# Optimization experiments

Measured on AMD Instinct MI355X. Metric: run time of the kernel, lower is better.

## Reference

```python
import jax, jax.numpy as jnp
import numpy as np

INPT, HID, NNODE, K, B = 64, 128, 10000, 16, 8

def setup_inputs() -> dict:
    key = jax.random.key(0)
    ks = jax.random.split(key, 12)
    def lin(k, fan_in, fan_out):
        # orthogonal-ish init stand-in; exact init values are irrelevant for the reference math
        return jax.random.normal(k, (fan_in, fan_out), jnp.float32) / np.sqrt(fan_in)
    return {
        "state": jax.random.normal(ks[0], (B, NNODE, INPT), jnp.float32),
        "internal": jax.random.normal(ks[1], (B, NNODE, INPT), jnp.float32),
        "state_neigh": jax.random.randint(ks[2], (NNODE, K), 0, NNODE),
        "internal_neigh": jax.random.randint(ks[3], (NNODE, K), 0, NNODE),
        "W1": lin(ks[4], INPT, HID), "b1": jnp.zeros((HID,), jnp.float32),
        "W2": lin(ks[5], HID, HID), "b2": jnp.zeros((HID,), jnp.float32),
        "Wu1": lin(ks[6], 2 * HID, HID), "bu1": jnp.zeros((HID,), jnp.float32),
        "Wu2": lin(ks[7], 2 * HID, HID), "bu2": jnp.zeros((HID,), jnp.float32),
    }

def _aggregate(se, ie, s_idx, i_idx):
    # se, ie: [B, N, H]; idx: [N, K] -> gather neighbors and sum over K
    g_s = jnp.take(se, s_idx, axis=1).sum(axis=2)   # [B, N, H]
    g_i = jnp.take(ie, i_idx, axis=1).sum(axis=2)   # [B, N, H]
    return g_s + g_i

def _update(aggr, h, W, b):
    x = jnp.concatenate((aggr, h), axis=-1)          # [B, N, 2H]
    return jax.nn.relu(x @ W + b)

def reference(state, internal, state_neigh, internal_neigh,
              W1, b1, W2, b2, Wu1, bu1, Wu2, bu2):
    # layer-1 embeddings
    state_embed = jax.nn.relu(state @ W1 + b1)       # [B, N, H]
    internal_embed = jax.nn.relu(internal @ W1 + b1)
    aggr1 = _aggregate(state_embed, internal_embed, state_neigh, internal_neigh)
    hu1 = _update(aggr1, internal_embed, Wu1, bu1)   # [B, N, H]
    # layer-2 embeddings
    se2 = jax.nn.relu(state_embed @ W2 + b2)
    ie2 = jax.nn.relu(hu1 @ W2 + b2)
    aggr2 = _aggregate(se2, ie2, state_neigh, internal_neigh)
    hu2 = _update(aggr2, ie2, Wu2, bu2)              # [B, N, H]
    return hu1, hu2
```

## Files before the change

kernel.cpp:

```cpp
#include <hip/hip_runtime.h>

#define HID 128
#define NNODE 10000
#define KN 16
#define ROWS 80000
#define NTILES 2500
#define ANCH 313

typedef __attribute__((ext_vector_type(8))) short short8;
typedef __attribute__((ext_vector_type(4))) float f32x4;
typedef __attribute__((ext_vector_type(2))) float f32x2;
typedef __attribute__((ext_vector_type(2))) unsigned int u32x2;

__device__ __forceinline__ unsigned short f2b(float f) {
    unsigned u = __float_as_uint(f);
    u += 0x7FFFu + ((u >> 16) & 1u);
    return (unsigned short)(u >> 16);
}

__global__ __launch_bounds__(256) void wconv_all(
    const float* __restrict__ W1, const float* __restrict__ W2,
    const float* __restrict__ Wu1, const float* __restrict__ Wu2,
    unsigned short* __restrict__ W1t, unsigned short* __restrict__ W2t,
    unsigned short* __restrict__ Wu1t, unsigned short* __restrict__ Wu2t) {
    int idx = blockIdx.x * 256 + threadIdx.x;
    const float* W; unsigned short* Wt; int K; int off;
    if (idx < 8192)       { W = W1;  Wt = W1t;  K = 64;  off = idx; }
    else if (idx < 24576) { W = W2;  Wt = W2t;  K = 128; off = idx - 8192; }
    else if (idx < 57344) { W = Wu1; Wt = Wu1t; K = 256; off = idx - 24576; }
    else                  { W = Wu2; Wt = Wu2t; K = 256; off = idx - 57344; }
    int n = off & 127, k = off >> 7;
    Wt[n * K + k] = f2b(W[off]);
}

template<int K, bool AF32>
__global__ __launch_bounds__(512) void embed2(
    const void* __restrict__ A0, const void* __restrict__ A1,
    const unsigned short* __restrict__ Wt, const float* __restrict__ bias,
    unsigned short* __restrict__ Y0, unsigned short* __restrict__ Y1, int tot) {
    const int t = threadIdx.x, w = t >> 6, lane = t & 63;
    const int lrow = lane & 15, lk = lane >> 4;
    const int rs = w & 1, ng = w >> 1;
    const int col0 = ng * 32;

    short8 wf[2][K / 32];
    f32x4 bv[2];
#pragma unroll
    for (int p = 0; p < 2; ++p) {
        bv[p] = *(const f32x4*)(bias + col0 + p * 16 + lk * 4);
#pragma unroll
        for (int kt = 0; kt < K / 32; ++kt)
            wf[p][kt] = *(const short8*)(Wt + (col0 + p * 16 + lrow) * K + kt * 32 + lk * 8);
    }

    int T = blockIdx.x;
    if (T >= tot) return;

    auto loadx = [&](int TT, short8* xf) {
        const int half = TT >= NTILES;
        const void* A = half ? A1 : A0;
        const int row = (TT - half * NTILES) * 32 + rs * 16 + lrow;
        if constexpr (AF32) {
            const float* X = (const float*)A + (size_t)row * K;
#pragma unroll
            for (int kt = 0; kt < K / 32; ++kt) {
                f32x4 f0 = *(const f32x4*)(X + kt * 32 + lk * 8);
                f32x4 f1 = *(const f32x4*)(X + kt * 32 + lk * 8 + 4);
                short8 v;
#pragma unroll
                for (int e = 0; e < 4; ++e) { v[e] = (short)f2b(f0[e]); v[4 + e] = (short)f2b(f1[e]); }
                xf[kt] = v;
            }
        } else {
            const unsigned short* X = (const unsigned short*)A + (size_t)row * K;
#pragma unroll
            for (int kt = 0; kt < K / 32; ++kt)
                xf[kt] = *(const short8*)(X + kt * 32 + lk * 8);
        }
    };

    short8 xf[K / 32], xn[K / 32];
    loadx(T, xf);
    for (;;) {
        const int Tn = T + gridDim.x;
        const bool more = Tn < tot;
        if (more) loadx(Tn, xn);

        const int half = T >= NTILES;
        unsigned short* Y = half ? Y1 : Y0;
        const int row = (T - half * NTILES) * 32 + rs * 16 + lrow;
#pragma unroll
        for (int p = 0; p < 2; ++p) {
            f32x4 acc = {0.f, 0.f, 0.f, 0.f};
#pragma unroll
            for (int kt = 0; kt < K / 32; ++kt)
                acc = __builtin_amdgcn_mfma_f32_16x16x32_bf16(wf[p][kt], xf[kt], acc, 0, 0, 0);
            float v0 = acc[0] + bv[p][0]; v0 = v0 > 0.f ? v0 : 0.f;
            float v1 = acc[1] + bv[p][1]; v1 = v1 > 0.f ? v1 : 0.f;
            float v2 = acc[2] + bv[p][2]; v2 = v2 > 0.f ? v2 : 0.f;
            float v3 = acc[3] + bv[p][3]; v3 = v3 > 0.f ? v3 : 0.f;
            u32x2 ov = {(unsigned)f2b(v0) | ((unsigned)f2b(v1) << 16),
                        (unsigned)f2b(v2) | ((unsigned)f2b(v3) << 16)};
            *(u32x2*)(Y + (size_t)row * HID + col0 + p * 16 + lk * 4) = ov;
        }
        if (!more) break;
#pragma unroll
        for (int kt = 0; kt < K / 32; ++kt) xf[kt] = xn[kt];
        T = Tn;
    }
}

__global__ __launch_bounds__(512) void aggr3(
    const unsigned short* __restrict__ SE, const unsigned short* __restrict__ IE,
    const int* __restrict__ sidx, const int* __restrict__ iidx,
    unsigned short* __restrict__ G) {
    __shared__ int sh[32][33];
    const int t = threadIdx.x;
    const int b = blockIdx.x & 7;
    const int hc = blockIdx.x >> 3;
    const int h = hc >= ANCH ? 1 : 0;
    const int c = hc - h * ANCH;
    const int n0 = c * 32;

#pragma unroll
    for (int q = 0; q < 2; ++q) {
        const int e = t + q * 512;
        const int r = e >> 5, k = e & 31;
        int nr = n0 + r; if (nr > NNODE - 1) nr = NNODE - 1;
        sh[r][k] = (k < KN) ? sidx[nr * KN + k] : iidx[nr * KN + (k - KN)];
    }
    __syncthreads();

    const int r = t >> 4, p = t & 15;
    const int col0 = h * 64 + p * 4;
    const int n = n0 + r;
    const size_t base = (size_t)b * NNODE * HID + col0;

    u32x2 vs[16], vi[16];
#pragma unroll
    for (int j = 0; j < 16; ++j)
        vs[j] = *(const u32x2*)(SE + base + (size_t)sh[r][j] * HID);
#pragma unroll
    for (int j = 0; j < 16; ++j)
        vi[j] = *(const u32x2*)(IE + base + (size_t)sh[r][16 + j] * HID);

    f32x2 a0 = {0.f, 0.f}, a1 = {0.f, 0.f};
#pragma unroll
    for (int j = 0; j < 16; ++j) {
        unsigned u0 = vs[j][0], u1 = vs[j][1];
        a0 += (f32x2){__uint_as_float(u0 << 16), __uint_as_float(u0 & 0xffff0000u)};
        a1 += (f32x2){__uint_as_float(u1 << 16), __uint_as_float(u1 & 0xffff0000u)};
    }
#pragma unroll
    for (int j = 0; j < 16; ++j) {
        unsigned u0 = vi[j][0], u1 = vi[j][1];
        a0 += (f32x2){__uint_as_float(u0 << 16), __uint_as_float(u0 & 0xffff0000u)};
        a1 += (f32x2){__uint_as_float(u1 << 16), __uint_as_float(u1 & 0xffff0000u)};
    }

    if (n < NNODE) {
        u32x2 ov = {(unsigned)f2b(a0.x) | ((unsigned)f2b(a0.y) << 16),
                    (unsigned)f2b(a1.x) | ((unsigned)f2b(a1.y) << 16)};
        *(u32x2*)(G + ((size_t)b * NNODE + n) * HID + col0) = ov;
    }
}

__global__ __launch_bounds__(512) void update_gemm2(
    const unsigned short* __restrict__ G, const unsigned short* __restrict__ H,
    const unsigned short* __restrict__ Wut, const float* __restrict__ bu,
    float* __restrict__ Yf, unsigned short* __restrict__ Yb, int writeb) {
    const int t = threadIdx.x, w = t >> 6, lane = t & 63;
    const int lrow = lane & 15, lk = lane >> 4;
    const int rs = w & 1, ng = w >> 1;
    const int col0 = ng * 32;

    short8 wf[2][8];
    f32x4 bv[2];
#pragma unroll
    for (int p = 0; p < 2; ++p) {
        bv[p] = *(const f32x4*)(bu + col0 + p * 16 + lk * 4);
#pragma unroll
        for (int kt = 0; kt < 8; ++kt)
            wf[p][kt] = *(const short8*)(Wut + (col0 + p * 16 + lrow) * 256 + kt * 32 + lk * 8);
    }

    for (int T = blockIdx.x; T < NTILES; T += gridDim.x) {
        const int row = T * 32 + rs * 16 + lrow;
        short8 xf[8];
#pragma unroll
        for (int kt = 0; kt < 4; ++kt) {
            xf[kt]     = *(const short8*)(G + (size_t)row * HID + kt * 32 + lk * 8);
            xf[4 + kt] = *(const short8*)(H + (size_t)row * HID + kt * 32 + lk * 8);
        }
#pragma unroll
        for (int p = 0; p < 2; ++p) {
            f32x4 acc = {0.f, 0.f, 0.f, 0.f};
#pragma unroll
            for (int kt = 0; kt < 8; ++kt)
                acc = __builtin_amdgcn_mfma_f32_16x16x32_bf16(wf[p][kt], xf[kt], acc, 0, 0, 0);
            f32x4 o;
#pragma unroll
            for (int j = 0; j < 4; ++j) {
                float v = acc[j] + bv[p][j];
                o[j] = v > 0.f ? v : 0.f;
            }
            *(f32x4*)(Yf + (size_t)row * HID + col0 + p * 16 + lk * 4) = o;
            if (writeb) {
                u32x2 ov = {(unsigned)f2b(o[0]) | ((unsigned)f2b(o[1]) << 16),
                            (unsigned)f2b(o[2]) | ((unsigned)f2b(o[3]) << 16)};
                *(u32x2*)(Yb + (size_t)row * HID + col0 + p * 16 + lk * 4) = ov;
            }
        }
    }
}

extern "C" void kernel_launch(void* const* d_in, const int* in_sizes, int n_in,
                              void* d_out, int out_size, void* d_ws, size_t ws_size,
                              hipStream_t stream) {
    const float* state    = (const float*)d_in[0];
    const float* internal = (const float*)d_in[1];
    const int*   sidx     = (const int*)d_in[2];
    const int*   iidx     = (const int*)d_in[3];
    const float* W1  = (const float*)d_in[4];
    const float* b1  = (const float*)d_in[5];
    const float* W2  = (const float*)d_in[6];
    const float* b2  = (const float*)d_in[7];
    const float* Wu1 = (const float*)d_in[8];
    const float* bu1 = (const float*)d_in[9];
    const float* Wu2 = (const float*)d_in[10];
    const float* bu2 = (const float*)d_in[11];

    float* hu1 = (float*)d_out;
    float* hu2 = hu1 + (size_t)ROWS * HID;

    unsigned short* W1t  = (unsigned short*)d_ws;
    unsigned short* W2t  = W1t  + 64 * 128;
    unsigned short* Wu1t = W2t  + 128 * 128;
    unsigned short* Wu2t = Wu1t + 256 * 128;
    unsigned short* bufA = Wu2t + 256 * 128;
    unsigned short* bufB = bufA + (size_t)ROWS * HID;
    unsigned short* bufC = bufB + (size_t)ROWS * HID;
    unsigned short* bufD = bufC + (size_t)ROWS * HID;

    const size_t need4 = (size_t)90112 * 2 + 4 * (size_t)ROWS * HID * 2;
    const bool big = ws_size >= need4;

    dim3 b256(256), b512(512);
    const int AGRID = 8 * 2 * ANCH;

    wconv_all<<<352, b256, 0, stream>>>(W1, W2, Wu1, Wu2, W1t, W2t, Wu1t, Wu2t);

    embed2<64, true><<<1250, b512, 0, stream>>>(state, internal, W1t, b1, bufA, bufB, 2 * NTILES);

    if (big) {
        aggr3<<<AGRID, b512, 0, stream>>>(bufA, bufB, sidx, iidx, bufD);
        update_gemm2<<<1250, b512, 0, stream>>>(bufD, bufB, Wu1t, bu1, hu1, bufC, 1);
        embed2<128, false><<<1250, b512, 0, stream>>>(bufA, bufC, W2t, b2, bufB, bufD, 2 * NTILES);
        aggr3<<<AGRID, b512, 0, stream>>>(bufB, bufD, sidx, iidx, bufA);
        update_gemm2<<<1250, b512, 0, stream>>>(bufA, bufD, Wu2t, bu2, hu2, nullptr, 0);
    } else {
        unsigned short* Ghu2 = (unsigned short*)hu2;
        aggr3<<<AGRID, b512, 0, stream>>>(bufA, bufB, sidx, iidx, Ghu2);
        update_gemm2<<<1250, b512, 0, stream>>>(Ghu2, bufB, Wu1t, bu1, hu1, bufC, 1);
        embed2<128, false><<<1250, b512, 0, stream>>>(bufA, nullptr, W2t, b2, bufB, nullptr, NTILES);
        embed2<128, false><<<1250, b512, 0, stream>>>(bufC, nullptr, W2t, b2, bufA, nullptr, NTILES);
        aggr3<<<AGRID, b512, 0, stream>>>(bufB, bufA, sidx, iidx, bufC);
        update_gemm2<<<1250, b512, 0, stream>>>(bufC, bufA, Wu2t, bu2, hu2, nullptr, 0);
    }
}
```

Before: 235.5 us.

## Fuse layer-2 embedding GEMM into embed1 and update1 kernels via LDS

The W2 embedding GEMM is folded into the producers of its inputs. The first-layer embed kernel also computes se2 for the state half. The first update kernel computes ie2 directly from hu1. Both stage the bf16 tile in an XOR-swizzled LDS buffer to re-layout it as MFMA operands. This drops a separate kernel launch and the global write/read round-trip of bf16 hu1 and the re-read of SE1. It also interleaves load and accumulate in the aggregation kernel to cut register pressure. The trade-offs: the embed kernel loses its software prefetch of the next tile, two __syncthreads are added per tile, and W2 fragments are reloaded from global/cache every tile.

Measured after the change: 237.9 us. Within noise of the previous version (+1.0%).

```diff
diff --git a/kernel.cpp b/kernel.cpp
--- a/kernel.cpp
+++ b/kernel.cpp
@@ -6,6 +6,7 @@
 #define ROWS 80000
 #define NTILES 2500
 #define ANCH 313
+#define AGRID (8 * 2 * ANCH)
 
 typedef __attribute__((ext_vector_type(8))) short short8;
 typedef __attribute__((ext_vector_type(4))) float f32x4;
@@ -33,84 +34,98 @@
     Wt[n * K + k] = f2b(W[off]);
 }
 
-template<int K, bool AF32>
-__global__ __launch_bounds__(512) void embed2(
-    const void* __restrict__ A0, const void* __restrict__ A1,
-    const unsigned short* __restrict__ Wt, const float* __restrict__ bias,
-    unsigned short* __restrict__ Y0, unsigned short* __restrict__ Y1, int tot) {
+__device__ __forceinline__ void lds_write8(unsigned short* Yt, int row, int bc, u32x2 v) {
+    *(u32x2*)((char*)Yt + row * 256 + (bc ^ ((row & 7) << 4))) = v;
+}
+__device__ __forceinline__ short8 lds_read16(const unsigned short* Yt, int row, int bc) {
+    return *(const short8*)((const char*)Yt + row * 256 + (bc ^ ((row & 7) << 4)));
+}
+
+__global__ __launch_bounds__(512) void k_embed1_fused(
+    const float* __restrict__ state, const float* __restrict__ internal,
+    const unsigned short* __restrict__ W1t, const float* __restrict__ b1,
+    const unsigned short* __restrict__ W2t, const float* __restrict__ b2,
+    unsigned short* __restrict__ SE1, unsigned short* __restrict__ IE1,
+    unsigned short* __restrict__ se2) {
+    __shared__ __align__(16) unsigned short Yt[32 * 128];
     const int t = threadIdx.x, w = t >> 6, lane = t & 63;
     const int lrow = lane & 15, lk = lane >> 4;
     const int rs = w & 1, ng = w >> 1;
     const int col0 = ng * 32;
-
-    short8 wf[2][K / 32];
-    f32x4 bv[2];
+    const int row_l = rs * 16 + lrow;
+
+    short8 wf[2][2];
+    f32x4 bv1[2], bv2[2];
 #pragma unroll
     for (int p = 0; p < 2; ++p) {
-        bv[p] = *(const f32x4*)(bias + col0 + p * 16 + lk * 4);
-#pragma unroll
-        for (int kt = 0; kt < K / 32; ++kt)
-            wf[p][kt] = *(const short8*)(Wt + (col0 + p * 16 + lrow) * K + kt * 32 + lk * 8);
-    }
-
-    int T = blockIdx.x;
-    if (T >= tot) return;
-
-    auto loadx = [&](int TT, short8* xf) {
-        const int half = TT >= NTILES;
-        const void* A = half ? A1 : A0;
-        const int row = (TT - half * NTILES) * 32 + rs * 16 + lrow;
-        if constexpr (AF32) {
-            const float* X = (const float*)A + (size_t)row * K;
-#pragma unroll
-            for (int kt = 0; kt < K / 32; ++kt) {
-                f32x4 f0 = *(const f32x4*)(X + kt * 32 + lk * 8);
-                f32x4 f1 = *(const f32x4*)(X + kt * 32 + lk * 8 + 4);
-                short8 v;
-#pragma unroll
-                for (int e = 0; e < 4; ++e) { v[e] = (short)f2b(f0[e]); v[4 + e] = (short)f2b(f1[e]); }
-                xf[kt] = v;
-            }
-        } else {
-            const unsigned short* X = (const unsigned short*)A + (size_t)row * K;
-#pragma unroll
-            for (int kt = 0; kt < K / 32; ++kt)
-                xf[kt] = *(const short8*)(X + kt * 32 + lk * 8);
-        }
-    };
-
-    short8 xf[K / 32], xn[K / 32];
-    loadx(T, xf);
-    for (;;) {
-        const int Tn = T + gridDim.x;
-        const bool more = Tn < tot;
-        if (more) loadx(Tn, xn);
-
+        bv1[p] = *(const f32x4*)(b1 + col0 + p * 16 + lk * 4);
+        bv2[p] = *(const f32x4*)(b2 + col0 + p * 16 + lk * 4);
+#pragma unroll
+        for (int kt = 0; kt < 2; ++kt)
+            wf[p][kt] = *(const short8*)(W1t + (col0 + p * 16 + lrow) * 64 + kt * 32 + lk * 8);
+    }
+
+    for (int T = blockIdx.x; T < 2 * NTILES; T += 1250) {
         const int half = T >= NTILES;
-        unsigned short* Y = half ? Y1 : Y0;
-        const int row = (T - half * NTILES) * 32 + rs * 16 + lrow;
+        const float* X = half ? internal : state;
+        unsigned short* Y = half ? IE1 : SE1;
+        const int row = (T - half * NTILES) * 32 + row_l;
+
+        short8 xf[2];
+#pragma unroll
+        for (int kt = 0; kt < 2; ++kt) {
+            const float* p4 = X + (size_t)row * 64 + kt * 32 + lk * 8;
+            f32x4 f0 = *(const f32x4*)p4;
+            f32x4 f1 = *(const f32x4*)(p4 + 4);
+            short8 v;
+#pragma unroll
+            for (int e = 0; e < 4; ++e) { v[e] = (short)f2b(f0[e]); v[4 + e] = (short)f2b(f1[e]); }
+            xf[kt] = v;
+        }
+
 #pragma unroll
         for (int p = 0; p < 2; ++p) {
             f32x4 acc = {0.f, 0.f, 0.f, 0.f};
-#pragma unroll
-            for (int kt = 0; kt < K / 32; ++kt)
-                acc = __builtin_amdgcn_mfma_f32_16x16x32_bf16(wf[p][kt], xf[kt], acc, 0, 0, 0);
-            float v0 = acc[0] + bv[p][0]; v0 = v0 > 0.f ? v0 : 0.f;
-            float v1 = acc[1] + bv[p][1]; v1 = v1 > 0.f ? v1 : 0.f;
-            float v2 = acc[2] + bv[p][2]; v2 = v2 > 0.f ? v2 : 0.f;
-            float v3 = acc[3] + bv[p][3]; v3 = v3 > 0.f ? v3 : 0.f;
+            acc = __builtin_amdgcn_mfma_f32_16x16x32_bf16(wf[p][0], xf[0], acc, 0, 0, 0);
+            acc = __builtin_amdgcn_mfma_f32_16x16x32_bf16(wf[p][1], xf[1], acc, 0, 0, 0);
+            float v0 = acc[0] + bv1[p][0]; v0 = v0 > 0.f ? v0 : 0.f;
+            float v1 = acc[1] + bv1[p][1]; v1 = v1 > 0.f ? v1 : 0.f;
+            float v2 = acc[2] + bv1[p][2]; v2 = v2 > 0.f ? v2 : 0.f;
+            float v3 = acc[3] + bv1[p][3]; v3 = v3 > 0.f ? v3 : 0.f;
             u32x2 ov = {(unsigned)f2b(v0) | ((unsigned)f2b(v1) << 16),
                         (unsigned)f2b(v2) | ((unsigned)f2b(v3) << 16)};
             *(u32x2*)(Y + (size_t)row * HID + col0 + p * 16 + lk * 4) = ov;
-        }
-        if (!more) break;
-#pragma unroll
-        for (int kt = 0; kt < K / 32; ++kt) xf[kt] = xn[kt];
-        T = Tn;
-    }
-}
-
-__global__ __launch_bounds__(512) void aggr3(
+            if (!half) lds_write8(Yt, row_l, col0 * 2 + p * 32 + lk * 8, ov);
+        }
+
+        if (!half) {
+            __syncthreads();
+            short8 x2[4];
+#pragma unroll
+            for (int kt = 0; kt < 4; ++kt)
+                x2[kt] = lds_read16(Yt, row_l, kt * 64 + lk * 16);
+            __syncthreads();
+#pragma unroll
+            for (int p = 0; p < 2; ++p) {
+                f32x4 acc = {0.f, 0.f, 0.f, 0.f};
+#pragma unroll
+                for (int kt = 0; kt < 4; ++kt) {
+                    short8 w2f = *(const short8*)(W2t + (col0 + p * 16 + lrow) * 128 + kt * 32 + lk * 8);
+                    acc = __builtin_amdgcn_mfma_f32_16x16x32_bf16(w2f, x2[kt], acc, 0, 0, 0);
+                }
+                float v0 = acc[0] + bv2[p][0]; v0 = v0 > 0.f ? v0 : 0.f;
+                float v1 = acc[1] + bv2[p][1]; v1 = v1 > 0.f ? v1 : 0.f;
+                float v2 = acc[2] + bv2[p][2]; v2 = v2 > 0.f ? v2 : 0.f;
+                float v3 = acc[3] + bv2[p][3]; v3 = v3 > 0.f ? v3 : 0.f;
+                u32x2 ov = {(unsigned)f2b(v0) | ((unsigned)f2b(v1) << 16),
+                            (unsigned)f2b(v2) | ((unsigned)f2b(v3) << 16)};
+                *(u32x2*)(se2 + (size_t)row * HID + col0 + p * 16 + lk * 4) = ov;
+            }
+        }
+    }
+}
+
+__global__ __launch_bounds__(512) void k_aggrD(
     const unsigned short* __restrict__ SE, const unsigned short* __restrict__ IE,
     const int* __restrict__ sidx, const int* __restrict__ iidx,
     unsigned short* __restrict__ G) {
@@ -136,26 +151,30 @@
     const int n = n0 + r;
     const size_t base = (size_t)b * NNODE * HID + col0;
 
-    u32x2 vs[16], vi[16];
-#pragma unroll
-    for (int j = 0; j < 16; ++j)
-        vs[j] = *(const u32x2*)(SE + base + (size_t)sh[r][j] * HID);
-#pragma unroll
-    for (int j = 0; j < 16; ++j)
-        vi[j] = *(const u32x2*)(IE + base + (size_t)sh[r][16 + j] * HID);
-
     f32x2 a0 = {0.f, 0.f}, a1 = {0.f, 0.f};
-#pragma unroll
-    for (int j = 0; j < 16; ++j) {
-        unsigned u0 = vs[j][0], u1 = vs[j][1];
-        a0 += (f32x2){__uint_as_float(u0 << 16), __uint_as_float(u0 & 0xffff0000u)};
-        a1 += (f32x2){__uint_as_float(u1 << 16), __uint_as_float(u1 & 0xffff0000u)};
-    }
-#pragma unroll
-    for (int j = 0; j < 16; ++j) {
-        unsigned u0 = vi[j][0], u1 = vi[j][1];
-        a0 += (f32x2){__uint_as_float(u0 << 16), __uint_as_float(u0 & 0xffff0000u)};
-        a1 += (f32x2){__uint_as_float(u1 << 16), __uint_as_float(u1 & 0xffff0000u)};
+    {
+        u32x2 vs[16];
+#pragma unroll
+        for (int j = 0; j < 16; ++j)
+            vs[j] = *(const u32x2*)(SE + base + (size_t)sh[r][j] * HID);
+#pragma unroll
+        for (int j = 0; j < 16; ++j) {
+            unsigned u0 = vs[j][0], u1 = vs[j][1];
+            a0 += (f32x2){__uint_as_float(u0 << 16), __uint_as_float(u0 & 0xffff0000u)};
+            a1 += (f32x2){__uint_as_float(u1 << 16), __uint_as_float(u1 & 0xffff0000u)};
+        }
+    }
+    {
+        u32x2 vi[16];
+#pragma unroll
+        for (int j = 0; j < 16; ++j)
+            vi[j] = *(const u32x2*)(IE + base + (size_t)sh[r][16 + j] * HID);
+#pragma unroll
+        for (int j = 0; j < 16; ++j) {
+            unsigned u0 = vi[j][0], u1 = vi[j][1];
+            a0 += (f32x2){__uint_as_float(u0 << 16), __uint_as_float(u0 & 0xffff0000u)};
+            a1 += (f32x2){__uint_as_float(u1 << 16), __uint_as_float(u1 & 0xffff0000u)};
+        }
     }
 
     if (n < NNODE) {
@@ -165,10 +184,84 @@
     }
 }
 
-__global__ __launch_bounds__(512) void update_gemm2(
+__global__ __launch_bounds__(512) void k_update1_fused(
+    const unsigned short* __restrict__ G, const unsigned short* __restrict__ H,
+    const unsigned short* __restrict__ Wu1t, const float* __restrict__ bu1,
+    const unsigned short* __restrict__ W2t, const float* __restrict__ b2,
+    float* __restrict__ hu1, unsigned short* __restrict__ ie2) {
+    __shared__ __align__(16) unsigned short Yt[32 * 128];
+    const int t = threadIdx.x, w = t >> 6, lane = t & 63;
+    const int lrow = lane & 15, lk = lane >> 4;
+    const int rs = w & 1, ng = w >> 1;
+    const int col0 = ng * 32;
+    const int row_l = rs * 16 + lrow;
+
+    short8 wf[2][8];
+    f32x4 bv[2], bv2[2];
+#pragma unroll
+    for (int p = 0; p < 2; ++p) {
+        bv[p]  = *(const f32x4*)(bu1 + col0 + p * 16 + lk * 4);
+        bv2[p] = *(const f32x4*)(b2  + col0 + p * 16 + lk * 4);
+#pragma unroll
+        for (int kt = 0; kt < 8; ++kt)
+            wf[p][kt] = *(const short8*)(Wu1t + (col0 + p * 16 + lrow) * 256 + kt * 32 + lk * 8);
+    }
+
+    for (int T = blockIdx.x; T < NTILES; T += 1250) {
+        const int row = T * 32 + row_l;
+        short8 xf[8];
+#pragma unroll
+        for (int kt = 0; kt < 4; ++kt) {
+            xf[kt]     = *(const short8*)(G + (size_t)row * HID + kt * 32 + lk * 8);
+            xf[4 + kt] = *(const short8*)(H + (size_t)row * HID + kt * 32 + lk * 8);
+        }
+#pragma unroll
+        for (int p = 0; p < 2; ++p) {
+            f32x4 acc = {0.f, 0.f, 0.f, 0.f};
+#pragma unroll
+            for (int kt = 0; kt < 8; ++kt)
+                acc = __builtin_amdgcn_mfma_f32_16x16x32_bf16(wf[p][kt], xf[kt], acc, 0, 0, 0);
+            f32x4 o;
+#pragma unroll
+            for (int j = 0; j < 4; ++j) {
+                float v = acc[j] + bv[p][j];
+                o[j] = v > 0.f ? v : 0.f;
+            }
+            *(f32x4*)(hu1 + (size_t)row * HID + col0 + p * 16 + lk * 4) = o;
+            u32x2 ov = {(unsigned)f2b(o[0]) | ((unsigned)f2b(o[1]) << 16),
+                        (unsigned)f2b(o[2]) | ((unsigned)f2b(o[3]) << 16)};
+            lds_write8(Yt, row_l, col0 * 2 + p * 32 + lk * 8, ov);
+        }
+
+        __syncthreads();
+        short8 x2[4];
+#pragma unroll
+        for (int kt = 0; kt < 4; ++kt)
+            x2[kt] = lds_read16(Yt, row_l, kt * 64 + lk * 16);
+        __syncthreads();
+#pragma unroll
+        for (int p = 0; p < 2; ++p) {
+            f32x4 acc = {0.f, 0.f, 0.f, 0.f};
+#pragma unroll
+            for (int kt = 0; kt < 4; ++kt) {
+                short8 w2f = *(const short8*)(W2t + (col0 + p * 16 + lrow) * 128 + kt * 32 + lk * 8);
+                acc = __builtin_amdgcn_mfma_f32_16x16x32_bf16(w2f, x2[kt], acc, 0, 0, 0);
+            }
+            float v0 = acc[0] + bv2[p][0]; v0 = v0 > 0.f ? v0 : 0.f;
+            float v1 = acc[1] + bv2[p][1]; v1 = v1 > 0.f ? v1 : 0.f;
+            float v2 = acc[2] + bv2[p][2]; v2 = v2 > 0.f ? v2 : 0.f;
+            float v3 = acc[3] + bv2[p][3]; v3 = v3 > 0.f ? v3 : 0.f;
+            u32x2 ov = {(unsigned)f2b(v0) | ((unsigned)f2b(v1) << 16),
+                        (unsigned)f2b(v2) | ((unsigned)f2b(v3) << 16)};
+            *(u32x2*)(ie2 + (size_t)row * HID + col0 + p * 16 + lk * 4) = ov;
+        }
+    }
+}
+
+__global__ __launch_bounds__(512) void k_update2(
     const unsigned short* __restrict__ G, const unsigned short* __restrict__ H,
     const unsigned short* __restrict__ Wut, const float* __restrict__ bu,
-    float* __restrict__ Yf, unsigned short* __restrict__ Yb, int writeb) {
+    float* __restrict__ Yf) {
     const int t = threadIdx.x, w = t >> 6, lane = t & 63;
     const int lrow = lane & 15, lk = lane >> 4;
     const int rs = w & 1, ng = w >> 1;
@@ -205,11 +298,6 @@
                 o[j] = v > 0.f ? v : 0.f;
             }
             *(f32x4*)(Yf + (size_t)row * HID + col0 + p * 16 + lk * 4) = o;
-            if (writeb) {
-                u32x2 ov = {(unsigned)f2b(o[0]) | ((unsigned)f2b(o[1]) << 16),
-                            (unsigned)f2b(o[2]) | ((unsigned)f2b(o[3]) << 16)};
-                *(u32x2*)(Yb + (size_t)row * HID + col0 + p * 16 + lk * 4) = ov;
-            }
         }
     }
 }
@@ -234,37 +322,31 @@
     float* hu2 = hu1 + (size_t)ROWS * HID;
 
     unsigned short* W1t  = (unsigned short*)d_ws;
-    unsigned short* W2t  = W1t  + 64 * 128;
-    unsigned short* Wu1t = W2t  + 128 * 128;
-    unsigned short* Wu2t = Wu1t + 256 * 128;
-    unsigned short* bufA = Wu2t + 256 * 128;
-    unsigned short* bufB = bufA + (size_t)ROWS * HID;
-    unsigned short* bufC = bufB + (size_t)ROWS * HID;
-    unsigned short* bufD = bufC + (size_t)ROWS * HID;
-
-    const size_t need4 = (size_t)90112 * 2 + 4 * (size_t)ROWS * HID * 2;
-    const bool big = ws_size >= need4;
+    unsigned short* W2t  = W1t + 8192;
+    unsigned short* Wu1t = W2t + 16384;
+    unsigned short* Wu2t = Wu1t + 32768;
+    unsigned short* buf0 = Wu2t + 32768;
+    unsigned short* buf1 = buf0 + (size_t)ROWS * HID;
+    unsigned short* buf2 = buf1 + (size_t)ROWS * HID;
+    unsigned short* buf3 = buf2 + (size_t)ROWS * HID;
+
+    const size_t need_big = ((size_t)90112 + 4 * (size_t)ROWS * HID) * 2;
+    const bool big = ws_size >= need_big;
 
     dim3 b256(256), b512(512);
-    const int AGRID = 8 * 2 * ANCH;
 
     wconv_all<<<352, b256, 0, stream>>>(W1, W2, Wu1, Wu2, W1t, W2t, Wu1t, Wu2t);
 
-    embed2<64, true><<<1250, b512, 0, stream>>>(state, internal, W1t, b1, bufA, bufB, 2 * NTILES);
-
-    if (big) {
-        aggr3<<<AGRID, b512, 0, stream>>>(bufA, bufB, sidx, iidx, bufD);
-        update_gemm2<<<1250, b512, 0, stream>>>(bufD, bufB, Wu1t, bu1, hu1, bufC, 1);
-        embed2<128, false><<<1250, b512, 0, stream>>>(bufA, bufC, W2t, b2, bufB, bufD, 2 * NTILES);
-        aggr3<<<AGRID, b512, 0, stream>>>(bufB, bufD, sidx, iidx, bufA);
-        update_gemm2<<<1250, b512, 0, stream>>>(bufA, bufD, Wu2t, bu2, hu2, nullptr, 0);
-    } else {
-        unsigned short* Ghu2 = (unsigned short*)hu2;
-        aggr3<<<AGRID, b512, 0, stream>>>(bufA, bufB, sidx, iidx, Ghu2);
-        update_gemm2<<<1250, b512, 0, stream>>>(Ghu2, bufB, Wu1t, bu1, hu1, bufC, 1);
-        embed2<128, false><<<1250, b512, 0, stream>>>(bufA, nullptr, W2t, b2, bufB, nullptr, NTILES);
-        embed2<128, false><<<1250, b512, 0, stream>>>(bufC, nullptr, W2t, b2, bufA, nullptr, NTILES);
-        aggr3<<<AGRID, b512, 0, stream>>>(bufB, bufA, sidx, iidx, bufC);
-        update_gemm2<<<1250, b512, 0, stream>>>(bufC, bufA, Wu2t, bu2, hu2, nullptr, 0);
-    }
-}
+    k_embed1_fused<<<1250, b512, 0, stream>>>(state, internal, W1t, b1, W2t, b2,
+                                              buf0, buf1, buf2);
+
+    unsigned short* G1 = big ? buf3 : (unsigned short*)hu2;
+
+    k_aggrD<<<AGRID, b512, 0, stream>>>(buf0, buf1, sidx, iidx, G1);
+
+    k_update1_fused<<<1250, b512, 0, stream>>>(G1, buf1, Wu1t, bu1, W2t, b2, hu1, buf0);
+
+    k_aggrD<<<AGRID, b512, 0, stream>>>(buf2, buf0, sidx, iidx, buf1);
+
+    k_update2<<<1250, b512, 0, stream>>>(buf1, buf0, Wu2t, bu2, hu2);
+}
```

## Stage neighbor gathers through LDS via direct global-to-LDS loads; prefetch update tiles

Applied to the files above, without the earlier changes.

Rewrites the aggregation kernel so the neighbor rows are copied straight into shared memory with global_load_lds. Each wave loads 4 neighbors across 8 row-pairs, the work runs in two phases of 16 nodes, and the sum is then read back from LDS per thread. The update GEMM gains software prefetching of the next tile's inputs and launches with half as many blocks, so each block processes two tiles. The aim is to raise memory-level parallelism in the gather and hide load latency in the GEMM, at the cost of 64KB of LDS per block and fewer resident blocks.

New measurement: 251.1 us. 1.07x slower.

```diff
diff --git a/kernel.cpp b/kernel.cpp
--- a/kernel.cpp
+++ b/kernel.cpp
@@ -6,10 +6,10 @@
 #define ROWS 80000
 #define NTILES 2500
 #define ANCH 313
+#define AGRID (8 * 2 * ANCH)
 
 typedef __attribute__((ext_vector_type(8))) short short8;
 typedef __attribute__((ext_vector_type(4))) float f32x4;
-typedef __attribute__((ext_vector_type(2))) float f32x2;
 typedef __attribute__((ext_vector_type(2))) unsigned int u32x2;
 
 __device__ __forceinline__ unsigned short f2b(float f) {
@@ -110,17 +110,21 @@
     }
 }
 
-__global__ __launch_bounds__(512) void aggr3(
+__global__ __launch_bounds__(512) void k_aggrL(
     const unsigned short* __restrict__ SE, const unsigned short* __restrict__ IE,
     const int* __restrict__ sidx, const int* __restrict__ iidx,
     unsigned short* __restrict__ G) {
     __shared__ int sh[32][33];
+    __shared__ __align__(16) unsigned short stage[8 * 32 * 2 * 64];
     const int t = threadIdx.x;
+    const int lane = t & 63, wv = t >> 6;
     const int b = blockIdx.x & 7;
     const int hc = blockIdx.x >> 3;
     const int h = hc >= ANCH ? 1 : 0;
     const int c = hc - h * ANCH;
     const int n0 = c * 32;
+    const size_t gbase = (size_t)b * NNODE * HID;
+    const int colbase = h * 64;
 
 #pragma unroll
     for (int q = 0; q < 2; ++q) {
@@ -131,37 +135,44 @@
     }
     __syncthreads();
 
-    const int r = t >> 4, p = t & 15;
-    const int col0 = h * 64 + p * 4;
-    const int n = n0 + r;
-    const size_t base = (size_t)b * NNODE * HID + col0;
-
-    u32x2 vs[16], vi[16];
-#pragma unroll
-    for (int j = 0; j < 16; ++j)
-        vs[j] = *(const u32x2*)(SE + base + (size_t)sh[r][j] * HID);
-#pragma unroll
-    for (int j = 0; j < 16; ++j)
-        vi[j] = *(const u32x2*)(IE + base + (size_t)sh[r][16 + j] * HID);
-
-    f32x2 a0 = {0.f, 0.f}, a1 = {0.f, 0.f};
-#pragma unroll
-    for (int j = 0; j < 16; ++j) {
-        unsigned u0 = vs[j][0], u1 = vs[j][1];
-        a0 += (f32x2){__uint_as_float(u0 << 16), __uint_as_float(u0 & 0xffff0000u)};
-        a1 += (f32x2){__uint_as_float(u1 << 16), __uint_as_float(u1 & 0xffff0000u)};
-    }
-#pragma unroll
-    for (int j = 0; j < 16; ++j) {
-        unsigned u0 = vi[j][0], u1 = vi[j][1];
-        a0 += (f32x2){__uint_as_float(u0 << 16), __uint_as_float(u0 & 0xffff0000u)};
-        a1 += (f32x2){__uint_as_float(u1 << 16), __uint_as_float(u1 & 0xffff0000u)};
-    }
-
-    if (n < NNODE) {
-        u32x2 ov = {(unsigned)f2b(a0.x) | ((unsigned)f2b(a0.y) << 16),
-                    (unsigned)f2b(a1.x) | ((unsigned)f2b(a1.y) << 16)};
-        *(u32x2*)(G + ((size_t)b * NNODE + n) * HID + col0) = ov;
+#pragma unroll
+    for (int ph = 0; ph < 2; ++ph) {
+        {
+            const unsigned short* SRC = (wv < 4) ? SE : IE;
+#pragma unroll
+            for (int pr = 0; pr < 8; ++pr) {
+#pragma unroll
+                for (int j = 0; j < 4; ++j) {
+                    const int nb = wv * 4 + j;
+                    const int rA = ph * 16 + pr * 2 + (lane >> 5);
+                    const int idx = sh[rA][nb];
+                    const unsigned short* gp = SRC + gbase + (size_t)idx * HID
+                                               + colbase + (lane & 31) * 2;
+                    unsigned short* lp = stage + (pr * 32 + nb) * 128;
+                    __builtin_amdgcn_global_load_lds(
+                        (const __attribute__((address_space(1))) void*)gp,
+                        (__attribute__((address_space(3))) void*)lp, 4, 0, 0);
+                }
+            }
+        }
+        __syncthreads();
+
+        const int r = t >> 5, cc = t & 31;
+        const int pr = r >> 1, ro = r & 1;
+        float a0 = 0.f, a1 = 0.f;
+        const unsigned* sp = (const unsigned*)stage + ((size_t)pr * 64 + ro) * 32 + cc;
+#pragma unroll
+        for (int nb = 0; nb < 32; ++nb) {
+            const unsigned u = sp[nb * 64];
+            a0 += __uint_as_float(u << 16);
+            a1 += __uint_as_float(u & 0xffff0000u);
+        }
+        const int n = n0 + ph * 16 + r;
+        if (n < NNODE) {
+            const unsigned ov = (unsigned)f2b(a0) | ((unsigned)f2b(a1) << 16);
+            *(unsigned*)(G + ((size_t)b * NNODE + n) * HID + colbase + cc * 2) = ov;
+        }
+        if (ph == 0) __syncthreads();
     }
 }
 
@@ -184,14 +195,25 @@
             wf[p][kt] = *(const short8*)(Wut + (col0 + p * 16 + lrow) * 256 + kt * 32 + lk * 8);
     }
 
-    for (int T = blockIdx.x; T < NTILES; T += gridDim.x) {
-        const int row = T * 32 + rs * 16 + lrow;
-        short8 xf[8];
+    auto loadx = [&](int TT, short8* xf) {
+        const int row = TT * 32 + rs * 16 + lrow;
 #pragma unroll
         for (int kt = 0; kt < 4; ++kt) {
             xf[kt]     = *(const short8*)(G + (size_t)row * HID + kt * 32 + lk * 8);
             xf[4 + kt] = *(const short8*)(H + (size_t)row * HID + kt * 32 + lk * 8);
         }
+    };
+
+    int T = blockIdx.x;
+    if (T >= NTILES) return;
+    short8 xf[8], xn[8];
+    loadx(T, xf);
+    for (;;) {
+        const int Tn = T + gridDim.x;
+        const bool more = Tn < NTILES;
+        if (more) loadx(Tn, xn);
+
+        const int row = T * 32 + rs * 16 + lrow;
 #pragma unroll
         for (int p = 0; p < 2; ++p) {
             f32x4 acc = {0.f, 0.f, 0.f, 0.f};
@@ -211,6 +233,10 @@
                 *(u32x2*)(Yb + (size_t)row * HID + col0 + p * 16 + lk * 4) = ov;
             }
         }
+        if (!more) break;
+#pragma unroll
+        for (int kt = 0; kt < 8; ++kt) xf[kt] = xn[kt];
+        T = Tn;
     }
 }
 
@@ -234,10 +260,10 @@
     float* hu2 = hu1 + (size_t)ROWS * HID;
 
     unsigned short* W1t  = (unsigned short*)d_ws;
-    unsigned short* W2t  = W1t  + 64 * 128;
-    unsigned short* Wu1t = W2t  + 128 * 128;
-    unsigned short* Wu2t = Wu1t + 256 * 128;
-    unsigned short* bufA = Wu2t + 256 * 128;
+    unsigned short* W2t  = W1t + 8192;
+    unsigned short* Wu1t = W2t + 16384;
+    unsigned short* Wu2t = Wu1t + 32768;
+    unsigned short* bufA = Wu2t + 32768;
     unsigned short* bufB = bufA + (size_t)ROWS * HID;
     unsigned short* bufC = bufB + (size_t)ROWS * HID;
     unsigned short* bufD = bufC + (size_t)ROWS * HID;
@@ -246,25 +272,28 @@
     const bool big = ws_size >= need4;
 
     dim3 b256(256), b512(512);
-    const int AGRID = 8 * 2 * ANCH;
 
     wconv_all<<<352, b256, 0, stream>>>(W1, W2, Wu1, Wu2, W1t, W2t, Wu1t, Wu2t);
 
-    embed2<64, true><<<1250, b512, 0, stream>>>(state, internal, W1t, b1, bufA, bufB, 2 * NTILES);
+    embed2<64, true><<<1250, b512, 0, stream>>>(state, internal, W1t, b1,
+                                                bufA, bufB, 2 * NTILES);
 
     if (big) {
-        aggr3<<<AGRID, b512, 0, stream>>>(bufA, bufB, sidx, iidx, bufD);
-        update_gemm2<<<1250, b512, 0, stream>>>(bufD, bufB, Wu1t, bu1, hu1, bufC, 1);
-        embed2<128, false><<<1250, b512, 0, stream>>>(bufA, bufC, W2t, b2, bufB, bufD, 2 * NTILES);
-        aggr3<<<AGRID, b512, 0, stream>>>(bufB, bufD, sidx, iidx, bufA);
-        update_gemm2<<<1250, b512, 0, stream>>>(bufA, bufD, Wu2t, bu2, hu2, nullptr, 0);
+        k_aggrL<<<AGRID, b512, 0, stream>>>(bufA, bufB, sidx, iidx, bufD);
+        update_gemm2<<<625, b512, 0, stream>>>(bufD, bufB, Wu1t, bu1, hu1, bufC, 1);
+        embed2<128, false><<<1250, b512, 0, stream>>>(bufA, bufC, W2t, b2,
+                                                      bufB, bufD, 2 * NTILES);
+        k_aggrL<<<AGRID, b512, 0, stream>>>(bufB, bufD, sidx, iidx, bufA);
+        update_gemm2<<<625, b512, 0, stream>>>(bufA, bufD, Wu2t, bu2, hu2, nullptr, 0);
     } else {
         unsigned short* Ghu2 = (unsigned short*)hu2;
-        aggr3<<<AGRID, b512, 0, stream>>>(bufA, bufB, sidx, iidx, Ghu2);
-        update_gemm2<<<1250, b512, 0, stream>>>(Ghu2, bufB, Wu1t, bu1, hu1, bufC, 1);
-        embed2<128, false><<<1250, b512, 0, stream>>>(bufA, nullptr, W2t, b2, bufB, nullptr, NTILES);
-        embed2<128, false><<<1250, b512, 0, stream>>>(bufC, nullptr, W2t, b2, bufA, nullptr, NTILES);
-        aggr3<<<AGRID, b512, 0, stream>>>(bufB, bufA, sidx, iidx, bufC);
-        update_gemm2<<<1250, b512, 0, stream>>>(bufC, bufA, Wu2t, bu2, hu2, nullptr, 0);
-    }
-}
+        k_aggrL<<<AGRID, b512, 0, stream>>>(bufA, bufB, sidx, iidx, Ghu2);
+        update_gemm2<<<625, b512, 0, stream>>>(Ghu2, bufB, Wu1t, bu1, hu1, bufC, 1);
+        embed2<128, false><<<1250, b512, 0, stream>>>(bufA, nullptr, W2t, b2,
+                                                      bufB, nullptr, NTILES);
+        embed2<128, false><<<1250, b512, 0, stream>>>(bufC, nullptr, W2t, b2,
+                                                      bufA, nullptr, NTILES);
+        k_aggrL<<<AGRID, b512, 0, stream>>>(bufB, bufA, sidx, iidx, bufC);
+        update_gemm2<<<625, b512, 0, stream>>>(bufC, bufA, Wu2t, bu2, hu2, nullptr, 0);
+    }
+}
```
